# Optimization experiments

Measured on AMD Instinct MI355X. Metric: run time of the kernel, lower is better.

Reference implementation:

```python
import jax, jax.numpy as jnp
import numpy as np

# Dimensions (see shape_source)
D = 12       # tree depth / number of levels
N = 32768    # nodes per level
L = 3        # label_size
K = 4        # nary (max children)
HID = 128    # hidden_size == dim_E == dim_rep
V = 50000    # word_vocab_size
LAYERS = 2   # stacked NaryTreeLSTM layers


def setup_inputs() -> dict:
    key = jax.random.key(0)
    ks = jax.random.split(key, 10)
    s = 0.02  # weight init scale
    tokens = jax.random.randint(ks[0], (D, N, L), 0, V)
    # child indices in [-1, N]; -1 = no child, 0 = zero init row, 1..N = prev-level node
    indices = jax.random.randint(ks[1], (D, N, K), 0, N + 2) - 1
    E = jax.random.normal(ks[2], (V, HID))  # torch.randn init
    lin_w = jax.random.normal(ks[3], (HID, L * HID)) * s
    lin_b = jnp.zeros((HID,), jnp.float32)
    Uf_w = jax.random.normal(ks[4], (LAYERS, K * HID, K * HID)) * s
    Uf_b = jnp.zeros((LAYERS, K * HID), jnp.float32)
    Uiuo_w = jax.random.normal(ks[5], (LAYERS, 3 * HID, K * HID)) * s
    Uiuo_b = jnp.zeros((LAYERS, 3 * HID), jnp.float32)
    W_w = jax.random.normal(ks[6], (LAYERS, 4 * HID, HID)) * s
    W_b = jnp.zeros((LAYERS, 4 * HID), jnp.float32)
    return dict(tokens=tokens, indices=indices, E=E, lin_w=lin_w, lin_b=lin_b,
                Uf_w=Uf_w, Uf_b=Uf_b, Uiuo_w=Uiuo_w, Uiuo_b=Uiuo_b, W_w=W_w, W_b=W_b)


def _tree_lstm_layer(x, indices, Uf_w, Uf_b, Uiuo_w, Uiuo_b, W_w, W_b):
    """x: [D,N,HID], indices: [D,N,K] in [-1,N]. Returns (hs, cs): [D,N,HID]."""
    d = HID

    def step(carry, inp):
        h_full, c_full = carry              # [1+N, d]; row 0 is the zero init state
        xl, idx = inp                       # [N, d], [N, K]
        mask = (idx != -1)
        safe = jnp.where(mask, idx, 0)
        h = h_full[safe]                    # [N, K, d] gather of child hidden states
        c = c_full[safe]                    # [N, K, d]
        m = mask.astype(xl.dtype)[..., None]
        Wx = xl @ W_w.T + W_b               # [N, 4d]
        Wf, Wi, Wu, Wo = Wx[:, :d], Wx[:, d:2 * d], Wx[:, 2 * d:3 * d], Wx[:, 3 * d:]
        h_flat = h.reshape(N, K * d)
        fk = jax.nn.sigmoid(Wf[:, None, :] + (h_flat @ Uf_w.T + Uf_b).reshape(N, K, d))
        f = jnp.sum(fk * c * m, axis=1)     # masked sum over children
        iuo = h_flat @ Uiuo_w.T + Uiuo_b    # [N, 3d]
        i = jax.nn.sigmoid(iuo[:, :d] + Wi)
        u = jnp.tanh(iuo[:, d:2 * d] + Wu)
        o = jax.nn.sigmoid(iuo[:, 2 * d:] + Wo)
        new_c = i * u + f
        new_h = o * jnp.tanh(new_c)
        zero = jnp.zeros((1, d), xl.dtype)
        new_carry = (jnp.concatenate([zero, new_h], 0), jnp.concatenate([zero, new_c], 0))
        return new_carry, (new_h, new_c)

    init = (jnp.zeros((1 + N, d), x.dtype), jnp.zeros((1 + N, d), x.dtype))
    _, (hs, cs) = jax.lax.scan(step, init, (x, indices))
    return hs, cs


def reference(tokens, indices, E, lin_w, lin_b, Uf_w, Uf_b, Uiuo_w, Uiuo_b, W_w, W_b):
    # TreeEmbeddingLayer: gather token embeddings, concat label slots, project to HID
    emb = E[tokens].reshape(D, N, L * HID) @ lin_w.T + lin_b  # [D, N, HID]
    t = emb
    cs = None
    for l in range(LAYERS):
        skip = t
        hs, cs = _tree_lstm_layer(t, indices, Uf_w[l], Uf_b[l], Uiuo_w[l], Uiuo_b[l], W_w[l], W_b[l])
        t = hs + skip  # residual over levels
    hx = jnp.tile(t[-1][None], (2, 1, 1))   # [2, N, HID]
    cx = jnp.tile(cs[-1][None], (2, 1, 1))  # [2, N, HID]
    return hx, cx
```

## Files before the change

kernel.cpp:

```cpp
#include <hip/hip_runtime.h>
#include <cstdint>
#include <cstddef>

#define DD 12
#define NNODE 32768
#define LTOK 3
#define KCH 4
#define HD 128
#define NC_STEP 896
#define KD_STEP 640
#define NC_EMB 128
#define KD_EMB 384

typedef unsigned short u16;
typedef __attribute__((ext_vector_type(8))) __bf16 bf16x8;
typedef __attribute__((ext_vector_type(4))) float f32x4;

__device__ __forceinline__ float bf2f(unsigned int u) {
  union { unsigned int i; float f; } v; v.i = (u & 0xffffu) << 16; return v.f;
}
__device__ __forceinline__ u16 f2bf(float f) {
  union { float f; unsigned int i; } v; v.f = f;
  unsigned int x = v.i;
  return (u16)((x + 0x7fffu + ((x >> 16) & 1u)) >> 16);
}
__device__ __forceinline__ float sigm(float x) { return 1.f / (1.f + __expf(-x)); }
__device__ __forceinline__ float tanh_fast(float x) { return 1.f - 2.f / (1.f + __expf(2.f * x)); }
__device__ __forceinline__ void async16(const void* g, void* l) {
  __builtin_amdgcn_global_load_lds((const __attribute__((address_space(1))) unsigned int*)g,
                                   (__attribute__((address_space(3))) unsigned int*)l, 16, 0, 0);
}

#define BM 256
#define BN 128
#define BK 64

__global__ __launch_bounds__(512, 2) void gemm8_k(
    const u16* __restrict__ Abf, const u16* __restrict__ Tbf,
    const int* __restrict__ gidx, const u16* __restrict__ B,
    const float* __restrict__ bias, u16* __restrict__ outb,
    const u16* __restrict__ zbuf)
{
  __shared__ u16 As[3][BM * BK];
  __shared__ u16 Bs[3][BN * BK];
  const int t = threadIdx.x;
  const int w = t >> 6;
  const int L = t & 63;
  const int q = L >> 4;
  const int lrow8 = L >> 3;
  const int sub = L & 7;
  const int swz = sub ^ lrow8;

  const int bid = blockIdx.x;
  const int wg = (bid & 7) * 112 + (bid >> 3);
  const int rt = wg / 7;
  const int ct = wg - rt * 7;
  const int row0 = rt * BM;
  const int col0 = ct * BN;

  const int wm = w >> 1;
  const int wn = w & 1;
  const int mrow = wm * 64;
  const int ncol = wn * 64;

  f32x4 acc[4][4];
#pragma unroll
  for (int a = 0; a < 4; ++a)
#pragma unroll
    for (int b = 0; b < 4; ++b)
      acc[a][b] = f32x4{0.f, 0.f, 0.f, 0.f};

  int4 cidx[4];
#pragma unroll
  for (int jj = 0; jj < 4; ++jj)
    cidx[jj] = *(const int4*)&gidx[(row0 + w * 32 + jj * 8 + lrow8) * KCH];

  auto stageAll = [&](const int k0, const int sel) {
#pragma unroll
    for (int jb = 0; jb < 2; ++jb) {
      const int r = w * 16 + jb * 8;
      async16(B + (size_t)(col0 + r + lrow8) * KD_STEP + k0 + swz * 8,
              &Bs[sel][r * BK]);
    }
#pragma unroll
    for (int jj = 0; jj < 4; ++jj) {
      const int rbase = w * 32 + jj * 8;
      const u16* src;
      if (k0 < 4 * HD) {
        const int id = ((const int*)&cidx[jj])[k0 >> 7];
        const u16* base = (id >= 1) ? (Abf + (size_t)(id - 1) * HD) : zbuf;
        src = base + (k0 & 127) + swz * 8;
      } else {
        src = Tbf + (size_t)(row0 + rbase + lrow8) * HD + (k0 - 4 * HD) + swz * 8;
      }
      async16(src, &As[sel][rbase * BK]);
    }
  };

  stageAll(0, 0);
  stageAll(64, 1);
  asm volatile("s_waitcnt vmcnt(6)" ::: "memory");
  __builtin_amdgcn_sched_barrier(0);
  __builtin_amdgcn_s_barrier();
  __builtin_amdgcn_sched_barrier(0);

  constexpr int NT = KD_STEP / BK;
#pragma unroll
  for (int tt = 0; tt < NT; ++tt) {
    const int rd = tt % 3;
    if (tt + 2 < NT) stageAll((tt + 2) * BK, (tt + 2) % 3);

    bf16x8 af[4][2], bfv[4][2];
#pragma unroll
    for (int mt = 0; mt < 4; ++mt)
#pragma unroll
      for (int ks = 0; ks < 2; ++ks)
        af[mt][ks] = *(const bf16x8*)&As[rd][(mrow + mt * 16 + (L & 15)) * BK +
                                            (((ks * 4 + q) ^ (L & 7)) * 8)];
#pragma unroll
    for (int nt = 0; nt < 4; ++nt)
#pragma unroll
      for (int ks = 0; ks < 2; ++ks)
        bfv[nt][ks] = *(const bf16x8*)&Bs[rd][(ncol + nt * 16 + (L & 15)) * BK +
                                             (((ks * 4 + q) ^ (L & 7)) * 8)];

    __builtin_amdgcn_s_setprio(1);
#pragma unroll
    for (int ks = 0; ks < 2; ++ks)
#pragma unroll
      for (int mt = 0; mt < 4; ++mt)
#pragma unroll
        for (int nt = 0; nt < 4; ++nt)
          acc[mt][nt] = __builtin_amdgcn_mfma_f32_16x16x32_bf16(
              af[mt][ks], bfv[nt][ks], acc[mt][nt], 0, 0, 0);
    __builtin_amdgcn_s_setprio(0);

    if (tt < NT - 1) {
      if (tt + 2 < NT) asm volatile("s_waitcnt vmcnt(6)" ::: "memory");
      else             asm volatile("s_waitcnt vmcnt(0)" ::: "memory");
      __builtin_amdgcn_sched_barrier(0);
      __builtin_amdgcn_s_barrier();
      __builtin_amdgcn_sched_barrier(0);
    }
  }

#pragma unroll
  for (int nt = 0; nt < 4; ++nt) {
    const int col = col0 + ncol + nt * 16 + (L & 15);
    const float bb = bias[col];
#pragma unroll
    for (int mt = 0; mt < 4; ++mt) {
#pragma unroll
      for (int i = 0; i < 4; ++i) {
        const int row = row0 + mrow + mt * 16 + q * 4 + i;
        outb[(size_t)row * NC_STEP + col] = f2bf(acc[mt][nt][i] + bb);
      }
    }
  }
}

__global__ __launch_bounds__(256) void gemm_emb_k(
    const u16* __restrict__ Ebf, const int* __restrict__ tokd,
    const u16* __restrict__ Lbf, const float* __restrict__ bias,
    float* __restrict__ outf, u16* __restrict__ outb)
{
  __shared__ u16 As[128 * 64];
  __shared__ u16 Bs[128 * 64];
  const int t = threadIdx.x;
  const int w = t >> 6;
  const int L = t & 63;
  const int q = L >> 4;
  const int lrow8 = L >> 3;
  const int sub = L & 7;
  const int swz = sub ^ lrow8;
  const int row0 = blockIdx.x * 128;

  f32x4 acc[4][4];
#pragma unroll
  for (int a = 0; a < 4; ++a)
#pragma unroll
    for (int b = 0; b < 4; ++b)
      acc[a][b] = f32x4{0.f, 0.f, 0.f, 0.f};

  const int mrow = (w & 1) * 64;
  const int ncol = (w >> 1) * 64;

  int4 cidx[4];
#pragma unroll
  for (int jj = 0; jj < 4; ++jj) {
    const int rit = w * 32 + jj * 8 + lrow8;
    cidx[jj].x = tokd[(row0 + rit) * LTOK + 0];
    cidx[jj].y = tokd[(row0 + rit) * LTOK + 1];
    cidx[jj].z = tokd[(row0 + rit) * LTOK + 2];
    cidx[jj].w = 0;
  }

#pragma unroll
  for (int k0 = 0; k0 < KD_EMB; k0 += 64) {
    __syncthreads();
#pragma unroll
    for (int jj = 0; jj < 4; ++jj) {
      const int id = ((const int*)&cidx[jj])[k0 >> 7];
      const u16* base = Ebf + (size_t)id * HD;
      const int rit = w * 32 + jj * 8 + lrow8;
      async16(base + (k0 & 127) + swz * 8, &As[(w * 32 + jj * 8) * 64]);
      async16(Lbf + (size_t)rit * KD_EMB + k0 + swz * 8, &Bs[(w * 32 + jj * 8) * 64]);
    }
    __syncthreads();
#pragma unroll
    for (int ks = 0; ks < 2; ++ks) {
      bf16x8 af[4], bfr[4];
      const int pc = ((ks * 4 + q) ^ (L & 7)) * 8;
#pragma unroll
      for (int mt = 0; mt < 4; ++mt)
        af[mt] = *(const bf16x8*)&As[(mrow + mt * 16 + (L & 15)) * 64 + pc];
#pragma unroll
      for (int nt = 0; nt < 4; ++nt)
        bfr[nt] = *(const bf16x8*)&Bs[(ncol + nt * 16 + (L & 15)) * 64 + pc];
#pragma unroll
      for (int mt = 0; mt < 4; ++mt)
#pragma unroll
        for (int nt = 0; nt < 4; ++nt)
          acc[mt][nt] = __builtin_amdgcn_mfma_f32_16x16x32_bf16(af[mt], bfr[nt], acc[mt][nt], 0, 0, 0);
    }
  }

#pragma unroll
  for (int nt = 0; nt < 4; ++nt) {
    const int col = ncol + nt * 16 + (L & 15);
    const float bb = bias[col];
#pragma unroll
    for (int mt = 0; mt < 4; ++mt) {
#pragma unroll
      for (int i = 0; i < 4; ++i) {
        const int row = row0 + mrow + mt * 16 + q * 4 + i;
        const float v = acc[mt][nt][i] + bb;
        outf[(size_t)row * NC_EMB + col] = v;
        outb[(size_t)row * NC_EMB + col] = f2bf(v);
      }
    }
  }
}

__global__ __launch_bounds__(256) void cell_k(
    const u16* __restrict__ pre, const int* __restrict__ idxs,
    const float* __restrict__ c_prev, float* __restrict__ c_cur,
    u16* __restrict__ h_cur, float* __restrict__ t_io, u16* __restrict__ tbf)
{
  const int g = blockIdx.x * 256 + threadIdx.x;
  const int r = g >> 7;
  const int j = g & 127;
  const u16* pr = pre + (size_t)r * NC_STEP;
  float f = 0.f;
#pragma unroll
  for (int k = 0; k < KCH; ++k) {
    const int id = idxs[r * KCH + k];
    const float cg = (id >= 1) ? c_prev[(size_t)(id - 1) * HD + j] : 0.f;
    f += sigm(bf2f(pr[k * HD + j])) * cg;
  }
  const float iv = sigm(bf2f(pr[4 * HD + j]));
  const float uv = tanh_fast(bf2f(pr[5 * HD + j]));
  const float ov = sigm(bf2f(pr[6 * HD + j]));
  const float cn = iv * uv + f;
  const float hv = ov * tanh_fast(cn);
  c_cur[g] = cn;
  h_cur[g] = f2bf(hv);
  const float tn = t_io[g] + hv;
  t_io[g] = tn;
  tbf[g] = f2bf(tn);
}

__global__ __launch_bounds__(256) void conv_k(const float* __restrict__ src,
                                              u16* __restrict__ dst, int n4)
{
  const int g = blockIdx.x * 256 + threadIdx.x;
  if (g < n4) {
    float4 v = ((const float4*)src)[g];
    ((ushort4*)dst)[g] = make_ushort4(f2bf(v.x), f2bf(v.y), f2bf(v.z), f2bf(v.w));
  }
}

__global__ __launch_bounds__(256) void prep_k(
    const float* __restrict__ Uf_w, const float* __restrict__ Uf_b,
    const float* __restrict__ Uiuo_w, const float* __restrict__ Uiuo_b,
    const float* __restrict__ W_w, const float* __restrict__ W_b,
    u16* __restrict__ Ubig, float* __restrict__ biasbig)
{
  const int l = blockIdx.y;
  const int e = blockIdx.x * 256 + threadIdx.x;
  const int c = e / KD_STEP;
  const int k = e % KD_STEP;
  float v;
  if (k < 512) {
    v = (c < 512) ? Uf_w[((size_t)l * 512 + c) * 512 + k]
                  : Uiuo_w[((size_t)l * 384 + (c - 512)) * 512 + k];
  } else {
    const int q = k - 512;
    const int wr = (c < 512) ? (c & 127) : (128 + (c - 512));
    v = W_w[((size_t)l * 512 + wr) * 128 + q];
  }
  Ubig[((size_t)l * 896 + c) * 640 + k] = f2bf(v);
  if (e < 896) {
    const float b = (e < 512)
        ? (Uf_b[l * 512 + e] + W_b[l * 512 + (e & 127)])
        : (Uiuo_b[l * 384 + (e - 512)] + W_b[l * 512 + 128 + (e - 512)]);
    biasbig[l * 896 + e] = b;
  }
}

__global__ __launch_bounds__(256) void fin_k(
    const float* __restrict__ t_fin, const float* __restrict__ c_fin,
    float* __restrict__ out)
{
  const size_t NH = (size_t)NNODE * HD;
  const size_t g = (size_t)blockIdx.x * 256 + threadIdx.x;
  const float h = t_fin[g];
  const float c = c_fin[g];
  out[g] = h;
  out[NH + g] = h;
  out[2 * NH + g] = c;
  out[3 * NH + g] = c;
}

extern "C" void kernel_launch(void* const* d_in, const int* in_sizes, int n_in,
                              void* d_out, int out_size, void* d_ws, size_t ws_size,
                              hipStream_t stream)
{
  (void)in_sizes; (void)n_in; (void)out_size; (void)ws_size;
  const int*   tokens  = (const int*)d_in[0];
  const int*   indices = (const int*)d_in[1];
  const float* E       = (const float*)d_in[2];
  const float* lin_w   = (const float*)d_in[3];
  const float* lin_b   = (const float*)d_in[4];
  const float* Uf_w    = (const float*)d_in[5];
  const float* Uf_b    = (const float*)d_in[6];
  const float* Uiuo_w  = (const float*)d_in[7];
  const float* Uiuo_b  = (const float*)d_in[8];
  const float* W_w     = (const float*)d_in[9];
  const float* W_b     = (const float*)d_in[10];
  float* out = (float*)d_out;

  const size_t NH = (size_t)NNODE * HD;

  char* ws = (char*)d_ws;
  size_t off = 0;
  auto alloc = [&](size_t bytes) -> void* {
    void* p = ws + off;
    off = (off + bytes + 255) & ~(size_t)255;
    return p;
  };
  u16*   Ubig    = (u16*)alloc((size_t)2 * 896 * 640 * 2);
  float* biasbig = (float*)alloc(2 * 896 * 4);
  u16*   Ebf     = (u16*)alloc((size_t)50000 * HD * 2);
  u16*   Lbf     = (u16*)alloc((size_t)HD * KD_EMB * 2);
  float* tslice  = (float*)alloc(NH * 4);
  u16*   tbf     = (u16*)alloc(NH * 2);
  u16*   h0a     = (u16*)alloc(NH * 2);
  u16*   h0b     = (u16*)alloc(NH * 2);
  u16*   h1a     = (u16*)alloc(NH * 2);
  u16*   h1b     = (u16*)alloc(NH * 2);
  float* c0a     = (float*)alloc(NH * 4);
  float* c0b     = (float*)alloc(NH * 4);
  float* c1a     = (float*)alloc(NH * 4);
  float* c1b     = (float*)alloc(NH * 4);
  u16*   pre     = (u16*)alloc((size_t)NNODE * NC_STEP * 2);
  u16*   zbuf    = (u16*)alloc(512);

  u16*   h0[2] = {h0a, h0b};
  u16*   h1[2] = {h1a, h1b};
  float* c0[2] = {c0a, c0b};
  float* c1[2] = {c1a, c1b};

  hipMemsetAsync(zbuf, 0, 512, stream);
  hipMemsetAsync(h0[0], 0, NH * 2, stream);
  hipMemsetAsync(h1[0], 0, NH * 2, stream);
  hipMemsetAsync(c0[0], 0, NH * 4, stream);
  hipMemsetAsync(c1[0], 0, NH * 4, stream);
  prep_k<<<dim3(2240, 2), 256, 0, stream>>>(Uf_w, Uf_b, Uiuo_w, Uiuo_b, W_w, W_b,
                                            Ubig, biasbig);
  conv_k<<<dim3((50000 * HD / 4 + 255) / 256), 256, 0, stream>>>(E, Ebf, 50000 * HD / 4);
  conv_k<<<dim3((HD * KD_EMB / 4 + 255) / 256), 256, 0, stream>>>(lin_w, Lbf, HD * KD_EMB / 4);

  for (int d = 0; d < DD; ++d) {
    const int ri = d & 1, wi = (d + 1) & 1;
    const int* idxd = indices + (size_t)d * NNODE * KCH;
    const int* tokd = tokens + (size_t)d * NNODE * LTOK;

    gemm_emb_k<<<dim3(NNODE / 128), 256, 0, stream>>>(
        Ebf, tokd, Lbf, lin_b, tslice, tbf);

    for (int l = 0; l < 2; ++l) {
      const u16*   hp = (l == 0) ? h0[ri] : h1[ri];
      u16*         hc = (l == 0) ? h0[wi] : h1[wi];
      const float* cp = (l == 0) ? c0[ri] : c1[ri];
      float*       cc = (l == 0) ? c0[wi] : c1[wi];
      const u16* Ul = Ubig + (size_t)l * 896 * 640;
      const float* bl = biasbig + l * 896;
      gemm8_k<<<dim3((NNODE / BM) * (NC_STEP / BN)), 512, 0, stream>>>(
          hp, tbf, idxd, Ul, bl, pre, zbuf);
      cell_k<<<dim3((int)(NH / 256)), 256, 0, stream>>>(
          pre, idxd, cp, cc, hc, tslice, tbf);
    }
  }
  fin_k<<<dim3((int)(NH / 256)), 256, 0, stream>>>(tslice, c1[0], out);
}
```

Measured before the change: 2.327 ms.

## Widen GEMM tile to 256 columns and read weights directly from global

The gathered GEMM now uses 256x256 tiles, with the weight matrix padded with zero rows to 1024 columns so four column tiles cover it. B fragments are loaded straight from global memory into registers instead of being staged through LDS. Each wave now holds a 128x64 accumulator. The goal is to reuse the gathered A rows across more columns, which means fewer blocks and less gather traffic. In exchange it computes on padding columns, roughly 14% extra MFMA work, raises register pressure, and exposes global-load latency on B.

```diff
diff --git a/kernel.cpp b/kernel.cpp
--- a/kernel.cpp
+++ b/kernel.cpp
@@ -11,6 +11,7 @@
 #define KD_STEP 640
 #define NC_EMB 128
 #define KD_EMB 384
+#define NCP 1024
 
 typedef unsigned short u16;
 typedef __attribute__((ext_vector_type(8))) __bf16 bf16x8;
@@ -32,7 +33,7 @@
 }
 
 #define BM 256
-#define BN 128
+#define BN 256
 #define BK 64
 
 __global__ __launch_bounds__(512, 2) void gemm8_k(
@@ -42,7 +43,6 @@
     const u16* __restrict__ zbuf)
 {
   __shared__ u16 As[3][BM * BK];
-  __shared__ u16 Bs[3][BN * BK];
   const int t = threadIdx.x;
   const int w = t >> 6;
   const int L = t & 63;
@@ -52,20 +52,20 @@
   const int swz = sub ^ lrow8;
 
   const int bid = blockIdx.x;
-  const int wg = (bid & 7) * 112 + (bid >> 3);
-  const int rt = wg / 7;
-  const int ct = wg - rt * 7;
+  const int wg = (bid & 7) * 64 + (bid >> 3);
+  const int rt = wg >> 2;
+  const int ct = wg & 3;
   const int row0 = rt * BM;
   const int col0 = ct * BN;
 
-  const int wm = w >> 1;
-  const int wn = w & 1;
-  const int mrow = wm * 64;
+  const int wm = w >> 2;
+  const int wn = w & 3;
+  const int mrow = wm * 128;
   const int ncol = wn * 64;
 
-  f32x4 acc[4][4];
-#pragma unroll
-  for (int a = 0; a < 4; ++a)
+  f32x4 acc[8][4];
+#pragma unroll
+  for (int a = 0; a < 8; ++a)
 #pragma unroll
     for (int b = 0; b < 4; ++b)
       acc[a][b] = f32x4{0.f, 0.f, 0.f, 0.f};
@@ -75,13 +75,7 @@
   for (int jj = 0; jj < 4; ++jj)
     cidx[jj] = *(const int4*)&gidx[(row0 + w * 32 + jj * 8 + lrow8) * KCH];
 
-  auto stageAll = [&](const int k0, const int sel) {
-#pragma unroll
-    for (int jb = 0; jb < 2; ++jb) {
-      const int r = w * 16 + jb * 8;
-      async16(B + (size_t)(col0 + r + lrow8) * KD_STEP + k0 + swz * 8,
-              &Bs[sel][r * BK]);
-    }
+  auto stageA = [&](const int k0, const int sel) {
 #pragma unroll
     for (int jj = 0; jj < 4; ++jj) {
       const int rbase = w * 32 + jj * 8;
@@ -97,9 +91,9 @@
     }
   };
 
-  stageAll(0, 0);
-  stageAll(64, 1);
-  asm volatile("s_waitcnt vmcnt(6)" ::: "memory");
+  stageA(0, 0);
+  stageA(64, 1);
+  asm volatile("s_waitcnt vmcnt(4)" ::: "memory");
   __builtin_amdgcn_sched_barrier(0);
   __builtin_amdgcn_s_barrier();
   __builtin_amdgcn_sched_barrier(0);
@@ -108,35 +102,38 @@
 #pragma unroll
   for (int tt = 0; tt < NT; ++tt) {
     const int rd = tt % 3;
-    if (tt + 2 < NT) stageAll((tt + 2) * BK, (tt + 2) % 3);
-
-    bf16x8 af[4][2], bfv[4][2];
-#pragma unroll
-    for (int mt = 0; mt < 4; ++mt)
-#pragma unroll
-      for (int ks = 0; ks < 2; ++ks)
-        af[mt][ks] = *(const bf16x8*)&As[rd][(mrow + mt * 16 + (L & 15)) * BK +
-                                            (((ks * 4 + q) ^ (L & 7)) * 8)];
-#pragma unroll
-    for (int nt = 0; nt < 4; ++nt)
-#pragma unroll
-      for (int ks = 0; ks < 2; ++ks)
-        bfv[nt][ks] = *(const bf16x8*)&Bs[rd][(ncol + nt * 16 + (L & 15)) * BK +
-                                             (((ks * 4 + q) ^ (L & 7)) * 8)];
-
-    __builtin_amdgcn_s_setprio(1);
+
+    bf16x8 bfv[2][4];
 #pragma unroll
     for (int ks = 0; ks < 2; ++ks)
 #pragma unroll
-      for (int mt = 0; mt < 4; ++mt)
+      for (int nt = 0; nt < 4; ++nt) {
+        const int col = col0 + ncol + nt * 16 + (L & 15);
+        bfv[ks][nt] = *(const bf16x8*)&B[(size_t)col * KD_STEP + tt * 64 + (ks * 4 + q) * 8];
+      }
+    __builtin_amdgcn_sched_barrier(0);
+    if (tt + 2 < NT) stageA((tt + 2) * 64, (tt + 2) % 3);
+    __builtin_amdgcn_sched_barrier(0);
+
+#pragma unroll
+    for (int ks = 0; ks < 2; ++ks) {
+      bf16x8 af[8];
+#pragma unroll
+      for (int mt = 0; mt < 8; ++mt)
+        af[mt] = *(const bf16x8*)&As[rd][(mrow + mt * 16 + (L & 15)) * BK +
+                                        (((ks * 4 + q) ^ (L & 7)) * 8)];
+      __builtin_amdgcn_s_setprio(1);
+#pragma unroll
+      for (int mt = 0; mt < 8; ++mt)
 #pragma unroll
         for (int nt = 0; nt < 4; ++nt)
           acc[mt][nt] = __builtin_amdgcn_mfma_f32_16x16x32_bf16(
-              af[mt][ks], bfv[nt][ks], acc[mt][nt], 0, 0, 0);
-    __builtin_amdgcn_s_setprio(0);
+              af[mt], bfv[ks][nt], acc[mt][nt], 0, 0, 0);
+      __builtin_amdgcn_s_setprio(0);
+    }
 
     if (tt < NT - 1) {
-      if (tt + 2 < NT) asm volatile("s_waitcnt vmcnt(6)" ::: "memory");
+      if (tt + 2 < NT) asm volatile("s_waitcnt vmcnt(4)" ::: "memory");
       else             asm volatile("s_waitcnt vmcnt(0)" ::: "memory");
       __builtin_amdgcn_sched_barrier(0);
       __builtin_amdgcn_s_barrier();
@@ -147,13 +144,15 @@
 #pragma unroll
   for (int nt = 0; nt < 4; ++nt) {
     const int col = col0 + ncol + nt * 16 + (L & 15);
-    const float bb = bias[col];
-#pragma unroll
-    for (int mt = 0; mt < 4; ++mt) {
-#pragma unroll
-      for (int i = 0; i < 4; ++i) {
-        const int row = row0 + mrow + mt * 16 + q * 4 + i;
-        outb[(size_t)row * NC_STEP + col] = f2bf(acc[mt][nt][i] + bb);
+    if (col < NC_STEP) {
+      const float bb = bias[col];
+#pragma unroll
+      for (int mt = 0; mt < 8; ++mt) {
+#pragma unroll
+        for (int i = 0; i < 4; ++i) {
+          const int row = row0 + mrow + mt * 16 + q * 4 + i;
+          outb[(size_t)row * NC_STEP + col] = f2bf(acc[mt][nt][i] + bb);
+        }
       }
     }
   }
@@ -299,7 +298,7 @@
     const int wr = (c < 512) ? (c & 127) : (128 + (c - 512));
     v = W_w[((size_t)l * 512 + wr) * 128 + q];
   }
-  Ubig[((size_t)l * 896 + c) * 640 + k] = f2bf(v);
+  Ubig[((size_t)l * NCP + c) * 640 + k] = f2bf(v);
   if (e < 896) {
     const float b = (e < 512)
         ? (Uf_b[l * 512 + e] + W_b[l * 512 + (e & 127)])
@@ -349,7 +348,7 @@
     off = (off + bytes + 255) & ~(size_t)255;
     return p;
   };
-  u16*   Ubig    = (u16*)alloc((size_t)2 * 896 * 640 * 2);
+  u16*   Ubig    = (u16*)alloc((size_t)2 * NCP * 640 * 2);
   float* biasbig = (float*)alloc(2 * 896 * 4);
   u16*   Ebf     = (u16*)alloc((size_t)50000 * HD * 2);
   u16*   Lbf     = (u16*)alloc((size_t)HD * KD_EMB * 2);
@@ -372,6 +371,7 @@
   float* c1[2] = {c1a, c1b};
 
   hipMemsetAsync(zbuf, 0, 512, stream);
+  hipMemsetAsync(Ubig, 0, (size_t)2 * NCP * 640 * 2, stream);
   hipMemsetAsync(h0[0], 0, NH * 2, stream);
   hipMemsetAsync(h1[0], 0, NH * 2, stream);
   hipMemsetAsync(c0[0], 0, NH * 4, stream);
@@ -394,9 +394,9 @@
       u16*         hc = (l == 0) ? h0[wi] : h1[wi];
       const float* cp = (l == 0) ? c0[ri] : c1[ri];
       float*       cc = (l == 0) ? c0[wi] : c1[wi];
-      const u16* Ul = Ubig + (size_t)l * 896 * 640;
+      const u16* Ul = Ubig + (size_t)l * NCP * 640;
       const float* bl = biasbig + l * 896;
-      gemm8_k<<<dim3((NNODE / BM) * (NC_STEP / BN)), 512, 0, stream>>>(
+      gemm8_k<<<dim3((NNODE / BM) * (NCP / BN)), 512, 0, stream>>>(
           hp, tbf, idxd, Ul, bl, pre, zbuf);
       cell_k<<<dim3((int)(NH / 256)), 256, 0, stream>>>(
           pre, idxd, cp, cc, hc, tslice, tbf);
```

After: 2.778 ms. 1.19x slower.
